# Kernel tuning notes

Hardware: AMD Instinct MI355X
Metric: run time of the kernel (lower is better)

The kernel has to match this reference:

```python
import jax, jax.numpy as jnp
import numpy as np

WS = 7          # window_size
NH = 8          # num_heads
EMB = 128       # embedding_dim
HD = EMB // NH  # head_dim
SCALE = HD ** -0.5
LN_EPS = 1e-5


def setup_inputs() -> dict:
    key = jax.random.key(0)
    ks = jax.random.split(key, 5)
    B, N, C = 64, 3136, EMB  # H = W = 56
    x = jax.random.normal(ks[0], (B, N, C), dtype=jnp.float32)
    ln_gamma = jnp.ones((C,), dtype=jnp.float32)
    ln_beta = jnp.zeros((C,), dtype=jnp.float32)
    w_qkv = jax.random.normal(ks[1], (C, 3 * C), dtype=jnp.float32) * (C ** -0.5)
    b_qkv = jax.random.normal(ks[2], (3 * C,), dtype=jnp.float32) * 0.02
    w_out = jax.random.normal(ks[3], (C, C), dtype=jnp.float32) * (C ** -0.5)
    b_out = jax.random.normal(ks[4], (C,), dtype=jnp.float32) * 0.02
    return {"x": x, "ln_gamma": ln_gamma, "ln_beta": ln_beta,
            "w_qkv": w_qkv, "b_qkv": b_qkv, "w_out": w_out, "b_out": b_out}


def reference(x, ln_gamma, ln_beta, w_qkv, b_qkv, w_out, b_out):
    B, N, C = x.shape
    H = int(np.sqrt(N))  # static
    Wd = H

    # LayerNorm over last dim
    mu = jnp.mean(x, axis=-1, keepdims=True)
    var = jnp.mean(jnp.square(x - mu), axis=-1, keepdims=True)
    xn = (x - mu) * jax.lax.rsqrt(var + LN_EPS) * ln_gamma + ln_beta

    # divide windows: [B,N,C] -> [B*nWh*nWw, WS*WS, C]
    nW = H // WS
    win = xn.reshape(B, nW, WS, nW, WS, C).transpose(0, 1, 3, 2, 4, 5)
    win = win.reshape(-1, WS * WS, C)

    # QKV projection
    qkv = win @ w_qkv + b_qkv                      # [nw, 49, 3C]
    qkv = qkv.reshape(-1, WS * WS, 3, NH, HD).transpose(2, 0, 3, 1, 4)
    q, k, v = qkv[0], qkv[1], qkv[2]               # [nw, NH, 49, HD]

    scores = jnp.einsum('whqd,whkd->whqk', q, k) * SCALE
    probs = jax.nn.softmax(scores, axis=-1)
    attn = jnp.einsum('whqk,whkd->whqd', probs, v) # [nw, NH, 49, HD]
    attn = attn.transpose(0, 2, 1, 3).reshape(-1, WS * WS, C)

    out = attn @ w_out + b_out                     # [nw, 49, C]

    # merge windows -> [B, H, W, C]
    out = out.reshape(B, nW, nW, WS, WS, C).transpose(0, 1, 3, 2, 4, 5)
    return out.reshape(B, H, Wd, C)
```

## Files before the change

kernel.cpp:

```cpp
#include <hip/hip_runtime.h>

typedef float floatx4 __attribute__((ext_vector_type(4)));
typedef __bf16 bf16x8 __attribute__((ext_vector_type(8)));
typedef unsigned short u16t;
typedef unsigned int u32t;

static __device__ __forceinline__ u16t f2bf(float f) {
  return __builtin_bit_cast(u16t, (__bf16)f);
}
static __device__ __forceinline__ float bf2f(u16t h) {
  return __uint_as_float((u32t)h << 16);
}

#define MFMA(A, B, C) __builtin_amdgcn_mfma_f32_16x16x32_bf16((A), (B), (C), 0, 0, 0)

__global__ void pack_weights_kernel(const float* __restrict__ wqkv,
                                    const float* __restrict__ wout,
                                    u16t* __restrict__ wq_p,
                                    u16t* __restrict__ wo_p) {
  int g = blockIdx.x * blockDim.x + threadIdx.x;
  int l = g & 63;
  int s = (g >> 6) & 3;
  int n = g >> 8;
  int kbase = 32 * s + ((l >> 4) * 8);
  int cl = l & 15;
  if (n < 24) {
    int col = 16 * n + cl;
    u16t* dst = wq_p + g * 8;
#pragma unroll
    for (int j = 0; j < 8; ++j) dst[j] = f2bf(wqkv[(kbase + j) * 384 + col]);
  } else {
    int col = 16 * (n - 24) + cl;
    u16t* dst = wo_p + (g - 24 * 256) * 8;
#pragma unroll
    for (int j = 0; j < 8; ++j) dst[j] = f2bf(wout[(kbase + j) * 128 + col]);
  }
}

__global__ __launch_bounds__(256, 3) void win_attn_kernel(
    const float* __restrict__ x, const float* __restrict__ gamma,
    const float* __restrict__ beta, const u16t* __restrict__ wq_p,
    const float* __restrict__ bqkv, const u16t* __restrict__ wo_p,
    const float* __restrict__ bout, float* __restrict__ out) {
  __shared__ u16t xnK[64][136];
  __shared__ u16t xv[128 * 72];
  __shared__ u16t qp[64][104];

  const int tid = threadIdx.x;
  const int lane = tid & 63;
  const int w = tid >> 6;
  const int llo = lane & 15;
  const int lhi = lane >> 4;

  const int wi = blockIdx.x;
  const int bimg = wi >> 6;
  const int widx = wi & 63;
  const int nwh = widx >> 3;
  const int nww = widx & 7;
  const int base_off = (((bimg * 56) + nwh * 7) * 56 + nww * 7) * 128;
  const float* xbase = x + base_off;

  for (int i = tid; i < 15 * 64; i += 256) {
    int r = 49 + (i >> 6), c = (i & 63) << 1;
    *(u32t*)&xnK[r][c] = 0;
    *(u32t*)&xv[r * 136 + c] = 0;
  }

  {
    const float g0 = gamma[2 * lane], g1 = gamma[2 * lane + 1];
    const float b0 = beta[2 * lane], b1 = beta[2 * lane + 1];
    for (int t = w; t < 49; t += 4) {
      int wr = t / 7, wc = t - wr * 7;
      const float* row = xbase + (wr * 56 + wc) * 128;
      float2 v = *(const float2*)(row + 2 * lane);
      float sm = v.x + v.y;
      float sq = v.x * v.x + v.y * v.y;
#pragma unroll
      for (int m = 1; m < 64; m <<= 1) {
        sm += __shfl_xor(sm, m);
        sq += __shfl_xor(sq, m);
      }
      float mean = sm * (1.f / 128.f);
      float var = sq * (1.f / 128.f) - mean * mean;
      float rs = rsqrtf(var + 1e-5f);
      float y0 = (v.x - mean) * rs * g0 + b0;
      float y1 = (v.y - mean) * rs * g1 + b1;
      u16t h0 = f2bf(y0), h1 = f2bf(y1);
      u16t l0 = f2bf(y0 - bf2f(h0)), l1 = f2bf(y1 - bf2f(h1));
      *(u32t*)&xnK[t][2 * lane] = (u32t)h0 | ((u32t)h1 << 16);
      *(u32t*)&xv[t * 136 + 2 * lane] = (u32t)l0 | ((u32t)l1 << 16);
    }
  }
  __syncthreads();

  const int rowA = 16 * w + llo;
  const int rowC = 16 * w + lhi * 4;
  const floatx4 z4 = {0.f, 0.f, 0.f, 0.f};

  bf16x8 a_hi[4], a_lo[4];
#pragma unroll
  for (int s = 0; s < 4; ++s) {
    a_hi[s] = *(const bf16x8*)&xnK[rowA][s * 32 + lhi * 8];
    a_lo[s] = *(const bf16x8*)&xv[rowA * 136 + s * 32 + lhi * 8];
  }
  __syncthreads();

#pragma unroll 2
  for (int h = 0; h < 8; ++h) {
    const u16t* pwk = wq_p + (((8 + h) * 4) * 64 + lane) * 8;
    const u16t* pwv = wq_p + (((16 + h) * 4) * 64 + lane) * 8;
    floatx4 ak = z4, av = z4;
#pragma unroll
    for (int s = 0; s < 4; ++s) {
      bf16x8 bk = *(const bf16x8*)(pwk + s * 512);
      bf16x8 bv = *(const bf16x8*)(pwv + s * 512);
      ak = MFMA(a_hi[s], bk, ak);
      ak = MFMA(a_lo[s], bk, ak);
      av = MFMA(a_hi[s], bv, av);
      av = MFMA(a_lo[s], bv, av);
    }
    float bk_ = bqkv[128 + h * 16 + llo];
    float bv_ = bqkv[256 + h * 16 + llo];
#pragma unroll
    for (int r = 0; r < 4; ++r)
      xnK[rowC + r][h * 16 + llo] = f2bf(ak[r] + bk_);
    ushort4 vv;
    vv.x = f2bf(av[0] + bv_);
    vv.y = f2bf(av[1] + bv_);
    vv.z = f2bf(av[2] + bv_);
    vv.w = f2bf(av[3] + bv_);
    *(ushort4*)&xv[(h * 16 + llo) * 72 + rowC] = vv;
  }
  __syncthreads();

  const float SEXP = 0.25f * 1.44269504088896340736f;
  floatx4 oc[8];
#pragma unroll
  for (int n = 0; n < 8; ++n) oc[n] = z4;
  bf16x8 bq[4];
#pragma unroll
  for (int s = 0; s < 4; ++s)
    bq[s] = *(const bf16x8*)(wq_p + (s * 64 + lane) * 8);

  float rsum[4];
#pragma unroll 1
  for (int p = 0; p < 4; ++p) {
#pragma unroll
    for (int hp = 0; hp < 2; ++hp) {
      const int h = 2 * p + hp;
      floatx4 aq = z4;
#pragma unroll
      for (int s = 0; s < 4; ++s) {
        aq = MFMA(a_hi[s], bq[s], aq);
        aq = MFMA(a_lo[s], bq[s], aq);
      }
      if (h < 7) {
        bf16x8 bqn[4];
#pragma unroll
        for (int s = 0; s < 4; ++s)
          bqn[s] = *(const bf16x8*)(wq_p + (((h + 1) * 4 + s) * 64 + lane) * 8);
#pragma unroll
        for (int s = 0; s < 4; ++s) bq[s] = bqn[s];
      }
      float bq_ = bqkv[h * 16 + llo];
#pragma unroll
      for (int r = 0; r < 4; ++r) {
        float qv = aq[r] + bq_;
        u16t qh = f2bf(qv);
        qp[rowC + r][llo] = qh;
        qp[rowC + r][16 + llo] = f2bf(qv - bf2f(qh));
      }
      bf16x8 kb[4], pvb[2];
      const int bcol = h * 16 + (lhi & 1) * 8;
#pragma unroll
      for (int n = 0; n < 4; ++n)
        kb[n] = *(const bf16x8*)&xnK[16 * n + llo][bcol];
#pragma unroll
      for (int s2 = 0; s2 < 2; ++s2)
        pvb[s2] = *(const bf16x8*)&xv[(h * 16 + llo) * 72 + s2 * 32 + lhi * 8];
      __asm__ volatile("s_waitcnt lgkmcnt(0)" ::: "memory");

      bf16x8 aqf = *(const bf16x8*)&qp[rowA][lhi * 8];
      floatx4 sc[4];
#pragma unroll
      for (int n = 0; n < 4; ++n) sc[n] = MFMA(aqf, kb[n], z4);

#pragma unroll
      for (int j = 0; j < 4; ++j) {
        float m0 = -3.0e38f;
#pragma unroll
        for (int n = 0; n < 4; ++n) {
          int c = 16 * n + llo;
          if (c < 49) m0 = fmaxf(m0, sc[n][j]);
        }
#pragma unroll
        for (int m = 1; m < 16; m <<= 1) m0 = fmaxf(m0, __shfl_xor(m0, m));
        float s0 = 0.f;
#pragma unroll
        for (int n = 0; n < 4; ++n) {
          int c = 16 * n + llo;
          float pe = (c < 49) ? exp2f((sc[n][j] - m0) * SEXP) : 0.f;
          sc[n][j] = pe;
          s0 += pe;
        }
#pragma unroll
        for (int m = 1; m < 16; m <<= 1) s0 += __shfl_xor(s0, m);
        rsum[j] = 1.f / s0;
      }
#pragma unroll
      for (int n = 0; n < 4; ++n)
#pragma unroll
        for (int j = 0; j < 4; ++j)
          qp[rowC + j][16 * n + llo] = f2bf(sc[n][j]);
      __asm__ volatile("s_waitcnt lgkmcnt(0)" ::: "memory");

      floatx4 ao = z4;
#pragma unroll
      for (int s2 = 0; s2 < 2; ++s2) {
        bf16x8 ap = *(const bf16x8*)&qp[rowA][s2 * 32 + lhi * 8];
        ao = MFMA(ap, pvb[s2], ao);
      }
#pragma unroll
      for (int r = 0; r < 4; ++r)
        qp[rowC + r][64 + hp * 16 + llo] = f2bf(ao[r] * rsum[r]);
    }
    __asm__ volatile("s_waitcnt lgkmcnt(0)" ::: "memory");
    bf16x8 apair = *(const bf16x8*)&qp[rowA][64 + lhi * 8];
#pragma unroll
    for (int n = 0; n < 8; ++n)
      oc[n] = MFMA(apair, *(const bf16x8*)(wo_p + ((n * 4 + p) * 64 + lane) * 8),
                   oc[n]);
  }

  float bo[8];
#pragma unroll
  for (int n = 0; n < 8; ++n) bo[n] = bout[16 * n + llo];
  float* obase = out + base_off;
#pragma unroll
  for (int r = 0; r < 4; ++r) {
    int t = rowC + r;
    if (t < 49) {
      int wr = t / 7, wc = t - wr * 7;
      float* orow = obase + (wr * 56 + wc) * 128;
#pragma unroll
      for (int n = 0; n < 8; ++n) orow[16 * n + llo] = oc[n][r] + bo[n];
    }
  }
}

extern "C" void kernel_launch(void* const* d_in, const int* in_sizes, int n_in,
                              void* d_out, int out_size, void* d_ws,
                              size_t ws_size, hipStream_t stream) {
  const float* x = (const float*)d_in[0];
  const float* ln_g = (const float*)d_in[1];
  const float* ln_b = (const float*)d_in[2];
  const float* w_qkv = (const float*)d_in[3];
  const float* b_qkv = (const float*)d_in[4];
  const float* w_out = (const float*)d_in[5];
  const float* b_out = (const float*)d_in[6];
  float* out = (float*)d_out;

  u16t* wq_p = (u16t*)d_ws;
  u16t* wo_p = wq_p + 24 * 256 * 8;

  hipLaunchKernelGGL(pack_weights_kernel, dim3(32), dim3(256), 0, stream,
                     w_qkv, w_out, wq_p, wo_p);
  hipLaunchKernelGGL(win_attn_kernel, dim3(4096), dim3(256), 0, stream, x,
                     ln_g, ln_b, wq_p, b_qkv, wo_p, b_out, out);
}
```

Before: 366.9 us.

## Software-pipeline per-head Q projection and drop softmax max reduction

Restructures the per-head attention loop so each iteration computes Q for the next head and prefetches the next head's K/V fragments from LDS while finishing the current head's softmax and PV. The row-max shuffle reduction is removed and exp is applied to unshifted scores, and the hi/lo MFMA accumulations are split into two independent chains. Together these aim to shorten the dependency chain and cut shuffle instructions per head. Dropping the max subtraction risks exp overflow for large scores, and the larger qp buffer adds LDS use.

```diff
diff --git a/kernel.cpp b/kernel.cpp
--- a/kernel.cpp
+++ b/kernel.cpp
@@ -44,7 +44,7 @@
     const float* __restrict__ bout, float* __restrict__ out) {
   __shared__ u16t xnK[64][136];
   __shared__ u16t xv[128 * 72];
-  __shared__ u16t qp[64][104];
+  __shared__ u16t qp[64][136];
 
   const int tid = threadIdx.x;
   const int lane = tid & 63;
@@ -131,105 +131,144 @@
     vv.w = f2bf(av[3] + bv_);
     *(ushort4*)&xv[(h * 16 + llo) * 72 + rowC] = vv;
   }
-  __syncthreads();
 
   const float SEXP = 0.25f * 1.44269504088896340736f;
-  floatx4 oc[8];
-#pragma unroll
-  for (int n = 0; n < 8; ++n) oc[n] = z4;
   bf16x8 bq[4];
 #pragma unroll
   for (int s = 0; s < 4; ++s)
     bq[s] = *(const bf16x8*)(wq_p + (s * 64 + lane) * 8);
-
-  float rsum[4];
+  {
+    floatx4 aq0 = z4, aq1 = z4;
+#pragma unroll
+    for (int s = 0; s < 4; ++s) {
+      aq0 = MFMA(a_hi[s], bq[s], aq0);
+      aq1 = MFMA(a_lo[s], bq[s], aq1);
+    }
+    float bq_ = bqkv[llo];
+#pragma unroll
+    for (int r = 0; r < 4; ++r) {
+      float qv = (aq0[r] + aq1[r]) + bq_;
+      u16t qh = f2bf(qv);
+      qp[rowC + r][64 + llo] = qh;
+      qp[rowC + r][80 + llo] = f2bf(qv - bf2f(qh));
+    }
+#pragma unroll
+    for (int s = 0; s < 4; ++s)
+      bq[s] = *(const bf16x8*)(wq_p + ((4 + s) * 64 + lane) * 8);
+  }
+  __syncthreads();
+
+  floatx4 oc[8];
+#pragma unroll
+  for (int n = 0; n < 8; ++n) oc[n] = z4;
+
+  bf16x8 kb[4], pvb[2];
+  {
+    const int bcol = (lhi & 1) * 8;
+#pragma unroll
+    for (int n = 0; n < 4; ++n)
+      kb[n] = *(const bf16x8*)&xnK[16 * n + llo][bcol];
+#pragma unroll
+    for (int s2 = 0; s2 < 2; ++s2)
+      pvb[s2] = *(const bf16x8*)&xv[llo * 72 + s2 * 32 + lhi * 8];
+  }
+
 #pragma unroll 1
-  for (int p = 0; p < 4; ++p) {
-#pragma unroll
-    for (int hp = 0; hp < 2; ++hp) {
-      const int h = 2 * p + hp;
-      floatx4 aq = z4;
+  for (int h = 0; h < 8; ++h) {
+    __asm__ volatile("s_waitcnt lgkmcnt(0)" ::: "memory");
+
+    bf16x8 aqf = *(const bf16x8*)&qp[rowA][64 + lhi * 8];
+    floatx4 sc[4];
+#pragma unroll
+    for (int n = 0; n < 4; ++n) sc[n] = MFMA(aqf, kb[n], z4);
+
+#pragma unroll
+    for (int n = 0; n < 4; ++n) {
+      int c = 16 * n + llo;
+#pragma unroll
+      for (int j = 0; j < 4; ++j)
+        sc[n][j] = (c < 49) ? exp2f(sc[n][j] * SEXP) : 0.f;
+    }
+#pragma unroll
+    for (int n = 0; n < 4; ++n)
+#pragma unroll
+      for (int j = 0; j < 4; ++j)
+        qp[rowC + j][16 * n + llo] = f2bf(sc[n][j]);
+
+    if (h < 7) {
+      floatx4 aq0 = z4, aq1 = z4;
 #pragma unroll
       for (int s = 0; s < 4; ++s) {
-        aq = MFMA(a_hi[s], bq[s], aq);
-        aq = MFMA(a_lo[s], bq[s], aq);
+        aq0 = MFMA(a_hi[s], bq[s], aq0);
+        aq1 = MFMA(a_lo[s], bq[s], aq1);
       }
-      if (h < 7) {
+      if (h < 6) {
         bf16x8 bqn[4];
 #pragma unroll
         for (int s = 0; s < 4; ++s)
-          bqn[s] = *(const bf16x8*)(wq_p + (((h + 1) * 4 + s) * 64 + lane) * 8);
+          bqn[s] = *(const bf16x8*)(wq_p + (((h + 2) * 4 + s) * 64 + lane) * 8);
 #pragma unroll
         for (int s = 0; s < 4; ++s) bq[s] = bqn[s];
       }
-      float bq_ = bqkv[h * 16 + llo];
+      float bq_ = bqkv[(h + 1) * 16 + llo];
 #pragma unroll
       for (int r = 0; r < 4; ++r) {
-        float qv = aq[r] + bq_;
+        float qv = (aq0[r] + aq1[r]) + bq_;
         u16t qh = f2bf(qv);
-        qp[rowC + r][llo] = qh;
-        qp[rowC + r][16 + llo] = f2bf(qv - bf2f(qh));
+        qp[rowC + r][64 + llo] = qh;
+        qp[rowC + r][80 + llo] = f2bf(qv - bf2f(qh));
       }
-      bf16x8 kb[4], pvb[2];
-      const int bcol = h * 16 + (lhi & 1) * 8;
+    }
+
+    float rsum[4];
+#pragma unroll
+    for (int j = 0; j < 4; ++j) {
+      float s0 = 0.f;
+#pragma unroll
+      for (int n = 0; n < 4; ++n) s0 += sc[n][j];
+#pragma unroll
+      for (int m = 1; m < 16; m <<= 1) s0 += __shfl_xor(s0, m);
+      rsum[j] = 1.f / s0;
+    }
+
+    if (h < 7) {
+      const int bcol = (h + 1) * 16 + (lhi & 1) * 8;
 #pragma unroll
       for (int n = 0; n < 4; ++n)
         kb[n] = *(const bf16x8*)&xnK[16 * n + llo][bcol];
+    }
+    bf16x8 pvc[2];
+#pragma unroll
+    for (int s2 = 0; s2 < 2; ++s2) pvc[s2] = pvb[s2];
+    if (h < 7) {
 #pragma unroll
       for (int s2 = 0; s2 < 2; ++s2)
-        pvb[s2] = *(const bf16x8*)&xv[(h * 16 + llo) * 72 + s2 * 32 + lhi * 8];
+        pvb[s2] =
+            *(const bf16x8*)&xv[((h + 1) * 16 + llo) * 72 + s2 * 32 + lhi * 8];
+    }
+    __asm__ volatile("s_waitcnt lgkmcnt(0)" ::: "memory");
+
+    floatx4 ao = z4;
+#pragma unroll
+    for (int s2 = 0; s2 < 2; ++s2) {
+      bf16x8 ap = *(const bf16x8*)&qp[rowA][s2 * 32 + lhi * 8];
+      ao = MFMA(ap, pvc[s2], ao);
+    }
+    const int hp = h & 1;
+#pragma unroll
+    for (int r = 0; r < 4; ++r)
+      qp[rowC + r][96 + hp * 16 + llo] = f2bf(ao[r] * rsum[r]);
+
+    if (hp) {
       __asm__ volatile("s_waitcnt lgkmcnt(0)" ::: "memory");
-
-      bf16x8 aqf = *(const bf16x8*)&qp[rowA][lhi * 8];
-      floatx4 sc[4];
-#pragma unroll
-      for (int n = 0; n < 4; ++n) sc[n] = MFMA(aqf, kb[n], z4);
-
-#pragma unroll
-      for (int j = 0; j < 4; ++j) {
-        float m0 = -3.0e38f;
-#pragma unroll
-        for (int n = 0; n < 4; ++n) {
-          int c = 16 * n + llo;
-          if (c < 49) m0 = fmaxf(m0, sc[n][j]);
-        }
-#pragma unroll
-        for (int m = 1; m < 16; m <<= 1) m0 = fmaxf(m0, __shfl_xor(m0, m));
-        float s0 = 0.f;
-#pragma unroll
-        for (int n = 0; n < 4; ++n) {
-          int c = 16 * n + llo;
-          float pe = (c < 49) ? exp2f((sc[n][j] - m0) * SEXP) : 0.f;
-          sc[n][j] = pe;
-          s0 += pe;
-        }
-#pragma unroll
-        for (int m = 1; m < 16; m <<= 1) s0 += __shfl_xor(s0, m);
-        rsum[j] = 1.f / s0;
-      }
-#pragma unroll
-      for (int n = 0; n < 4; ++n)
-#pragma unroll
-        for (int j = 0; j < 4; ++j)
-          qp[rowC + j][16 * n + llo] = f2bf(sc[n][j]);
-      __asm__ volatile("s_waitcnt lgkmcnt(0)" ::: "memory");
-
-      floatx4 ao = z4;
-#pragma unroll
-      for (int s2 = 0; s2 < 2; ++s2) {
-        bf16x8 ap = *(const bf16x8*)&qp[rowA][s2 * 32 + lhi * 8];
-        ao = MFMA(ap, pvb[s2], ao);
-      }
-#pragma unroll
-      for (int r = 0; r < 4; ++r)
-        qp[rowC + r][64 + hp * 16 + llo] = f2bf(ao[r] * rsum[r]);
-    }
-    __asm__ volatile("s_waitcnt lgkmcnt(0)" ::: "memory");
-    bf16x8 apair = *(const bf16x8*)&qp[rowA][64 + lhi * 8];
-#pragma unroll
-    for (int n = 0; n < 8; ++n)
-      oc[n] = MFMA(apair, *(const bf16x8*)(wo_p + ((n * 4 + p) * 64 + lane) * 8),
-                   oc[n]);
+      bf16x8 apair = *(const bf16x8*)&qp[rowA][96 + lhi * 8];
+      const int p = h >> 1;
+#pragma unroll
+      for (int n = 0; n < 8; ++n)
+        oc[n] = MFMA(apair,
+                     *(const bf16x8*)(wo_p + ((n * 4 + p) * 64 + lane) * 8),
+                     oc[n]);
+    }
   }
 
   float bo[8];
```

Result: faster. 355.7 us (-3.1%).

## Keep attention probabilities in registers via transposed MFMA operands and drop softmax max

Applied to the files above, without the earlier changes.

Swaps the A/B operands of the score, K-projection and PV MFMAs so that softmax probabilities and per-head attention outputs land directly in the register layout the next MFMA needs. This removes the LDS round trips through the old qp buffer and several lgkmcnt waits per head. The softmax row max is no longer subtracted, Q is projected with only the hi part of the split input, and next-head K/V/Q loads are software-prefetched. LDS use shrinks and launch bounds rise to 4 blocks per CU. In exchange, skipping max subtraction risks exp overflow on large scores, and the precision of Q drops slightly.

```diff
diff --git a/kernel.cpp b/kernel.cpp
--- a/kernel.cpp
+++ b/kernel.cpp
@@ -1,7 +1,9 @@
 #include <hip/hip_runtime.h>
 
 typedef float floatx4 __attribute__((ext_vector_type(4)));
+typedef __bf16 bf16t;
 typedef __bf16 bf16x8 __attribute__((ext_vector_type(8)));
+typedef __bf16 bf16x4 __attribute__((ext_vector_type(4)));
 typedef unsigned short u16t;
 typedef unsigned int u32t;
 
@@ -22,9 +24,9 @@
   int l = g & 63;
   int s = (g >> 6) & 3;
   int n = g >> 8;
-  int kbase = 32 * s + ((l >> 4) * 8);
   int cl = l & 15;
   if (n < 24) {
+    int kbase = 32 * s + ((l >> 4) * 8);
     int col = 16 * n + cl;
     u16t* dst = wq_p + g * 8;
 #pragma unroll
@@ -32,19 +34,21 @@
   } else {
     int col = 16 * (n - 24) + cl;
     u16t* dst = wo_p + (g - 24 * 256) * 8;
-#pragma unroll
-    for (int j = 0; j < 8; ++j) dst[j] = f2bf(wout[(kbase + j) * 128 + col]);
-  }
-}
-
-__global__ __launch_bounds__(256, 3) void win_attn_kernel(
+    int rbase = 32 * s + 4 * (l >> 4);
+#pragma unroll
+    for (int j = 0; j < 8; ++j)
+      dst[j] = f2bf(wout[(rbase + 16 * (j >> 2) + (j & 3)) * 128 + col]);
+  }
+}
+
+__global__ __launch_bounds__(256, 4) void win_attn_kernel(
     const float* __restrict__ x, const float* __restrict__ gamma,
     const float* __restrict__ beta, const u16t* __restrict__ wq_p,
     const float* __restrict__ bqkv, const u16t* __restrict__ wo_p,
     const float* __restrict__ bout, float* __restrict__ out) {
   __shared__ u16t xnK[64][136];
-  __shared__ u16t xv[128 * 72];
-  __shared__ u16t qp[64][104];
+  __shared__ u16t xv[9216];
+  __shared__ u16t qs[64][40];
 
   const int tid = threadIdx.x;
   const int lane = tid & 63;
@@ -114,16 +118,19 @@
     for (int s = 0; s < 4; ++s) {
       bf16x8 bk = *(const bf16x8*)(pwk + s * 512);
       bf16x8 bv = *(const bf16x8*)(pwv + s * 512);
-      ak = MFMA(a_hi[s], bk, ak);
-      ak = MFMA(a_lo[s], bk, ak);
+      ak = MFMA(bk, a_hi[s], ak);
+      ak = MFMA(bk, a_lo[s], ak);
       av = MFMA(a_hi[s], bv, av);
       av = MFMA(a_lo[s], bv, av);
     }
-    float bk_ = bqkv[128 + h * 16 + llo];
+    float4 bk4 = *(const float4*)(bqkv + 128 + h * 16 + 4 * lhi);
+    ushort4 kk;
+    kk.x = f2bf(ak[0] + bk4.x);
+    kk.y = f2bf(ak[1] + bk4.y);
+    kk.z = f2bf(ak[2] + bk4.z);
+    kk.w = f2bf(ak[3] + bk4.w);
+    *(ushort4*)&xnK[16 * w + llo][h * 16 + 4 * lhi] = kk;
     float bv_ = bqkv[256 + h * 16 + llo];
-#pragma unroll
-    for (int r = 0; r < 4; ++r)
-      xnK[rowC + r][h * 16 + llo] = f2bf(ak[r] + bk_);
     ushort4 vv;
     vv.x = f2bf(av[0] + bv_);
     vv.y = f2bf(av[1] + bv_);
@@ -131,104 +138,137 @@
     vv.w = f2bf(av[3] + bv_);
     *(ushort4*)&xv[(h * 16 + llo) * 72 + rowC] = vv;
   }
+
+  {
+    floatx4 aq = z4;
+#pragma unroll
+    for (int s = 0; s < 4; ++s) {
+      bf16x8 bq0 = *(const bf16x8*)(wq_p + (s * 64 + lane) * 8);
+      aq = MFMA(bq0, a_hi[s], aq);
+    }
+    float4 bq4 = *(const float4*)(bqkv + 4 * lhi);
+    ushort4 qhv, qlv;
+    float q0 = aq[0] + bq4.x, q1 = aq[1] + bq4.y;
+    float q2 = aq[2] + bq4.z, q3 = aq[3] + bq4.w;
+    qhv.x = f2bf(q0); qhv.y = f2bf(q1); qhv.z = f2bf(q2); qhv.w = f2bf(q3);
+    qlv.x = f2bf(q0 - bf2f(qhv.x));
+    qlv.y = f2bf(q1 - bf2f(qhv.y));
+    qlv.z = f2bf(q2 - bf2f(qhv.z));
+    qlv.w = f2bf(q3 - bf2f(qhv.w));
+    *(ushort4*)&qs[16 * w + llo][4 * lhi] = qhv;
+    *(ushort4*)&qs[16 * w + llo][16 + 4 * lhi] = qlv;
+  }
   __syncthreads();
+
+  bf16x8 kb[4];
+  bf16x4 v00, v01, v10, v11;
+  {
+    const int bcol = (lhi & 1) * 8;
+#pragma unroll
+    for (int n = 0; n < 4; ++n)
+      kb[n] = *(const bf16x8*)&xnK[16 * n + llo][bcol];
+    const int vrow = llo * 72;
+    v00 = *(const bf16x4*)&xv[vrow + 4 * lhi];
+    v01 = *(const bf16x4*)&xv[vrow + 16 + 4 * lhi];
+    v10 = *(const bf16x4*)&xv[vrow + 32 + 4 * lhi];
+    v11 = *(const bf16x4*)&xv[vrow + 48 + 4 * lhi];
+  }
 
   const float SEXP = 0.25f * 1.44269504088896340736f;
   floatx4 oc[8];
 #pragma unroll
   for (int n = 0; n < 8; ++n) oc[n] = z4;
-  bf16x8 bq[4];
-#pragma unroll
-  for (int s = 0; s < 4; ++s)
-    bq[s] = *(const bf16x8*)(wq_p + (s * 64 + lane) * 8);
-
-  float rsum[4];
+
 #pragma unroll 1
-  for (int p = 0; p < 4; ++p) {
+  for (int p4 = 0; p4 < 4; ++p4) {
+    bf16x8 atf;
 #pragma unroll
     for (int hp = 0; hp < 2; ++hp) {
-      const int h = 2 * p + hp;
-      floatx4 aq = z4;
-#pragma unroll
-      for (int s = 0; s < 4; ++s) {
-        aq = MFMA(a_hi[s], bq[s], aq);
-        aq = MFMA(a_lo[s], bq[s], aq);
-      }
+      const int h = 2 * p4 + hp;
+      bf16x8 bqn0, bqn1, bqn2, bqn3;
       if (h < 7) {
-        bf16x8 bqn[4];
-#pragma unroll
-        for (int s = 0; s < 4; ++s)
-          bqn[s] = *(const bf16x8*)(wq_p + (((h + 1) * 4 + s) * 64 + lane) * 8);
-#pragma unroll
-        for (int s = 0; s < 4; ++s) bq[s] = bqn[s];
-      }
-      float bq_ = bqkv[h * 16 + llo];
-#pragma unroll
-      for (int r = 0; r < 4; ++r) {
-        float qv = aq[r] + bq_;
-        u16t qh = f2bf(qv);
-        qp[rowC + r][llo] = qh;
-        qp[rowC + r][16 + llo] = f2bf(qv - bf2f(qh));
-      }
-      bf16x8 kb[4], pvb[2];
-      const int bcol = h * 16 + (lhi & 1) * 8;
-#pragma unroll
-      for (int n = 0; n < 4; ++n)
-        kb[n] = *(const bf16x8*)&xnK[16 * n + llo][bcol];
-#pragma unroll
-      for (int s2 = 0; s2 < 2; ++s2)
-        pvb[s2] = *(const bf16x8*)&xv[(h * 16 + llo) * 72 + s2 * 32 + lhi * 8];
+        const u16t* pq = wq_p + (((h + 1) * 4) * 64 + lane) * 8;
+        bqn0 = *(const bf16x8*)(pq);
+        bqn1 = *(const bf16x8*)(pq + 512);
+        bqn2 = *(const bf16x8*)(pq + 1024);
+        bqn3 = *(const bf16x8*)(pq + 1536);
+      }
       __asm__ volatile("s_waitcnt lgkmcnt(0)" ::: "memory");
 
-      bf16x8 aqf = *(const bf16x8*)&qp[rowA][lhi * 8];
+      bf16x8 aqf = *(const bf16x8*)&qs[16 * w + llo][8 * lhi];
       floatx4 sc[4];
 #pragma unroll
-      for (int n = 0; n < 4; ++n) sc[n] = MFMA(aqf, kb[n], z4);
-
-#pragma unroll
-      for (int j = 0; j < 4; ++j) {
-        float m0 = -3.0e38f;
-#pragma unroll
-        for (int n = 0; n < 4; ++n) {
-          int c = 16 * n + llo;
-          if (c < 49) m0 = fmaxf(m0, sc[n][j]);
-        }
-#pragma unroll
-        for (int m = 1; m < 16; m <<= 1) m0 = fmaxf(m0, __shfl_xor(m0, m));
-        float s0 = 0.f;
-#pragma unroll
-        for (int n = 0; n < 4; ++n) {
-          int c = 16 * n + llo;
-          float pe = (c < 49) ? exp2f((sc[n][j] - m0) * SEXP) : 0.f;
+      for (int n = 0; n < 4; ++n) sc[n] = MFMA(kb[n], aqf, z4);
+
+      if (h < 7) {
+        floatx4 aq = MFMA(bqn0, a_hi[0], z4);
+        aq = MFMA(bqn1, a_hi[1], aq);
+        aq = MFMA(bqn2, a_hi[2], aq);
+        aq = MFMA(bqn3, a_hi[3], aq);
+        float4 bq4 = *(const float4*)(bqkv + (h + 1) * 16 + 4 * lhi);
+        float q0 = aq[0] + bq4.x, q1 = aq[1] + bq4.y;
+        float q2 = aq[2] + bq4.z, q3 = aq[3] + bq4.w;
+        ushort4 qhv, qlv;
+        qhv.x = f2bf(q0); qhv.y = f2bf(q1); qhv.z = f2bf(q2); qhv.w = f2bf(q3);
+        qlv.x = f2bf(q0 - bf2f(qhv.x));
+        qlv.y = f2bf(q1 - bf2f(qhv.y));
+        qlv.z = f2bf(q2 - bf2f(qhv.z));
+        qlv.w = f2bf(q3 - bf2f(qhv.w));
+        *(ushort4*)&qs[16 * w + llo][4 * lhi] = qhv;
+        *(ushort4*)&qs[16 * w + llo][16 + 4 * lhi] = qlv;
+      }
+
+      float s0 = 0.f;
+#pragma unroll
+      for (int n = 0; n < 4; ++n) {
+#pragma unroll
+        for (int j = 0; j < 4; ++j) {
+          float pe;
+          if (n == 3)
+            pe = (4 * lhi + j < 1) ? exp2f(sc[n][j] * SEXP) : 0.f;
+          else
+            pe = exp2f(sc[n][j] * SEXP);
           sc[n][j] = pe;
           s0 += pe;
         }
-#pragma unroll
-        for (int m = 1; m < 16; m <<= 1) s0 += __shfl_xor(s0, m);
-        rsum[j] = 1.f / s0;
-      }
-#pragma unroll
-      for (int n = 0; n < 4; ++n)
-#pragma unroll
-        for (int j = 0; j < 4; ++j)
-          qp[rowC + j][16 * n + llo] = f2bf(sc[n][j]);
-      __asm__ volatile("s_waitcnt lgkmcnt(0)" ::: "memory");
-
-      floatx4 ao = z4;
-#pragma unroll
-      for (int s2 = 0; s2 < 2; ++s2) {
-        bf16x8 ap = *(const bf16x8*)&qp[rowA][s2 * 32 + lhi * 8];
-        ao = MFMA(ap, pvb[s2], ao);
-      }
-#pragma unroll
-      for (int r = 0; r < 4; ++r)
-        qp[rowC + r][64 + hp * 16 + llo] = f2bf(ao[r] * rsum[r]);
-    }
-    __asm__ volatile("s_waitcnt lgkmcnt(0)" ::: "memory");
-    bf16x8 apair = *(const bf16x8*)&qp[rowA][64 + lhi * 8];
+      }
+      s0 += __shfl_xor(s0, 16);
+      s0 += __shfl_xor(s0, 32);
+      float rq = 1.f / s0;
+
+      bf16x8 PB0, PB1;
+#pragma unroll
+      for (int j = 0; j < 4; ++j) {
+        PB0[j] = (bf16t)sc[0][j];
+        PB0[4 + j] = (bf16t)sc[1][j];
+        PB1[j] = (bf16t)sc[2][j];
+        PB1[4 + j] = (bf16t)sc[3][j];
+      }
+      bf16x8 V0 = __builtin_shufflevector(v00, v01, 0, 1, 2, 3, 4, 5, 6, 7);
+      bf16x8 V1 = __builtin_shufflevector(v10, v11, 0, 1, 2, 3, 4, 5, 6, 7);
+      floatx4 ao = MFMA(V0, PB0, z4);
+      ao = MFMA(V1, PB1, ao);
+      atf[4 * hp + 0] = (bf16t)(ao[0] * rq);
+      atf[4 * hp + 1] = (bf16t)(ao[1] * rq);
+      atf[4 * hp + 2] = (bf16t)(ao[2] * rq);
+      atf[4 * hp + 3] = (bf16t)(ao[3] * rq);
+
+      if (h < 7) {
+        const int bcol = (h + 1) * 16 + (lhi & 1) * 8;
+#pragma unroll
+        for (int n = 0; n < 4; ++n)
+          kb[n] = *(const bf16x8*)&xnK[16 * n + llo][bcol];
+        const int vrow = ((h + 1) * 16 + llo) * 72;
+        v00 = *(const bf16x4*)&xv[vrow + 4 * lhi];
+        v01 = *(const bf16x4*)&xv[vrow + 16 + 4 * lhi];
+        v10 = *(const bf16x4*)&xv[vrow + 32 + 4 * lhi];
+        v11 = *(const bf16x4*)&xv[vrow + 48 + 4 * lhi];
+      }
+    }
 #pragma unroll
     for (int n = 0; n < 8; ++n)
-      oc[n] = MFMA(apair, *(const bf16x8*)(wo_p + ((n * 4 + p) * 64 + lane) * 8),
+      oc[n] = MFMA(atf,
+                   *(const bf16x8*)(wo_p + ((n * 4 + p4) * 64 + lane) * 8),
                    oc[n]);
   }
 
```

Result: faster. 310.7 us (-15.3%).
